# Kernel tuning notes

Measured on AMD Instinct MI355X. Metric: run time of the kernel, lower is better.

The kernel has to match this reference:

```python
import jax, jax.numpy as jnp
import numpy as np

N = 20000      # n_nodes
E = 320000     # n_edges (avg degree 16)
DIM = 64       # feature dim
HEADS = 4      # attention heads; per-head channel = DIM (PyG TransformerConv with concat=False)


def setup_inputs() -> dict:
    key = jax.random.key(0)
    ks = jax.random.split(key, 12)
    s = 0.05
    return {
        "f_mole": jax.random.normal(ks[0], (N, DIM), jnp.float32),
        "edge_weight": jax.random.uniform(ks[1], (E,), jnp.float32),
        "gcn_w": jax.random.normal(ks[2], (DIM, DIM), jnp.float32) * s,
        "gcn_b": jnp.zeros((DIM,), jnp.float32),
        "wq": jax.random.normal(ks[3], (DIM, HEADS * DIM), jnp.float32) * s,
        "bq": jnp.zeros((HEADS * DIM,), jnp.float32),
        "wk": jax.random.normal(ks[4], (DIM, HEADS * DIM), jnp.float32) * s,
        "bk": jnp.zeros((HEADS * DIM,), jnp.float32),
        "wv": jax.random.normal(ks[5], (DIM, HEADS * DIM), jnp.float32) * s,
        "bv": jnp.zeros((HEADS * DIM,), jnp.float32),
        "wskip": jax.random.normal(ks[6], (DIM, DIM), jnp.float32) * s,
        "bskip": jnp.zeros((DIM,), jnp.float32),
        "wbeta": jax.random.normal(ks[7], (3 * DIM, 1), jnp.float32) * s,
        "conv_w": jax.random.normal(ks[8], (DIM, DIM), jnp.float32) * s,  # Conv1d weight[o,0,k,0]
        "conv_b": jnp.zeros((DIM,), jnp.float32),
        "edges": jax.random.randint(ks[9], (2, E), 0, N, jnp.int32),
    }


def _forward(f_mole, edge_weight, gcn_w, gcn_b, wq, bq, wk, bk, wv, bv,
             wskip, bskip, wbeta, conv_w, conv_b, edges):
    n = f_mole.shape[0]
    dim = f_mole.shape[1]
    heads = wq.shape[1] // dim
    src, dst = edges[0], edges[1]  # PyG flow: source -> target

    # ---- GCNConv(dim, dim) with edge weights (add_self_loops=True, normalize=True) ----
    loops = jnp.arange(n, dtype=src.dtype)
    src_sl = jnp.concatenate([src, loops])
    dst_sl = jnp.concatenate([dst, loops])
    ew = jnp.concatenate([edge_weight, jnp.ones((n,), f_mole.dtype)])
    deg = jax.ops.segment_sum(ew, dst_sl, num_segments=n)
    dinv = jnp.where(deg > 0, jax.lax.rsqrt(deg), 0.0)
    norm = dinv[src_sl] * ew * dinv[dst_sl]              # (E+N,)
    xw = f_mole @ gcn_w                                   # (N, dim)
    agg = jax.ops.segment_sum(norm[:, None] * xw[src_sl], dst_sl, num_segments=n)
    f_gcn = jax.nn.relu(agg + gcn_b)                      # (N, dim)

    # ---- TransformerConv(dim, dim, heads, concat=False, beta=True) ----
    q = (f_gcn @ wq + bq).reshape(n, heads, dim)
    k = (f_gcn @ wk + bk).reshape(n, heads, dim)
    v = (f_gcn @ wv + bv).reshape(n, heads, dim)
    logits = jnp.einsum('ehc,ehc->eh', q[dst], k[src]) / jnp.sqrt(jnp.float32(dim))  # (E, H)
    m = jax.ops.segment_max(logits, dst, num_segments=n)  # (N, H)
    ex = jnp.exp(logits - m[dst])
    z = jax.ops.segment_sum(ex, dst, num_segments=n)      # (N, H)
    alpha = ex / z[dst]                                   # per-target softmax over edges
    out = jax.ops.segment_sum(alpha[:, :, None] * v[src], dst, num_segments=n)  # (N, H, dim)
    out = out.mean(axis=1)                                # concat=False -> head mean
    x_r = f_gcn @ wskip + bskip                           # root/skip branch
    beta = jax.nn.sigmoid(jnp.concatenate([out, x_r, out - x_r], axis=-1) @ wbeta)  # (N, 1)
    f_tf = jax.nn.relu(beta * x_r + (1.0 - beta) * out)   # (N, dim)

    # ---- Conv1d(1, dim, kernel_size=(dim,1)) on f_tf.T viewed as (1,1,dim,N) ----
    # out[o, n] = sum_k conv_w[o, k] * f_tf.T[k, n] + conv_b[o]  -> shape (1, dim, 1, N)
    conv = jnp.einsum('ok,nk->on', conv_w, f_tf) + conv_b[:, None]  # (dim, N)
    # torch .view(1, n_mole, -1) on (1, dim, 1, N): row-major reshape
    f_intra = conv.reshape(1, n, dim)
    return f_intra


def reference(f_mole, edge_weight, gcn_w, gcn_b, wq, bq, wk, bk, wv, bv,
              wskip, bskip, wbeta, conv_w, conv_b, edges):
    return _forward(f_mole, edge_weight, gcn_w, gcn_b, wq, bq, wk, bk, wv, bv,
                    wskip, bskip, wbeta, conv_w, conv_b, edges)
```

## Files before the change

kernel.cpp:

```cpp
#include <hip/hip_runtime.h>
#include <hip/hip_bf16.h>
#include <hip/hip_fp16.h>

#define DIM 64
#define HEADS 4
#define HD 256
#define CAP 64

typedef __attribute__((ext_vector_type(8))) short bf16x8;
typedef __attribute__((ext_vector_type(8))) unsigned short u16x8;
typedef __attribute__((ext_vector_type(4))) float f32x4;

template<int CTRL>
__device__ __forceinline__ float dpp_rot(float x) {
    return __int_as_float(__builtin_amdgcn_update_dpp(
        0, __float_as_int(x), CTRL, 0xF, 0xF, true));
}
__device__ __forceinline__ float reduce16(float x) {
    x += dpp_rot<0x121>(x);
    x += dpp_rot<0x122>(x);
    x += dpp_rot<0x124>(x);
    x += dpp_rot<0x128>(x);
    return x;
}
__device__ __forceinline__ unsigned short f2bf(float f) {
    unsigned u = __float_as_uint(f);
    unsigned r = (u + 0x7FFFu + ((u >> 16) & 1u)) >> 16;
    return (unsigned short)r;
}
__device__ __forceinline__ float bf2f(unsigned short u) {
    return __uint_as_float((unsigned)u << 16);
}
__device__ __forceinline__ float rec_w(unsigned rec) {
    return __half2float(__ushort_as_half((unsigned short)(rec & 0xffffu)));
}

__global__ void scatter_all(const int* __restrict__ edges, const float* __restrict__ ew,
                            int* counts, unsigned* __restrict__ csr, int nE) {
    int e = blockIdx.x * blockDim.x + threadIdx.x;
    if (e < nE) {
        int dst = edges[nE + e];
        int src = edges[e];
        float w = ew[e];
        int p = atomicAdd(&counts[dst], 1);
        unsigned rec = ((unsigned)src << 16)
                     | (unsigned)__half_as_ushort(__float2half(w));
        csr[(dst << 6) + p] = rec;
    }
}

__global__ __launch_bounds__(256) void wt_conv(const float* __restrict__ wq,
                                               const float* __restrict__ wk,
                                               const float* __restrict__ wv,
                                               const float* __restrict__ wsk,
                                               unsigned short* __restrict__ wt) {
    int p = blockIdx.x;
    const float* W; int ncw, col0;
    if (p < 4)       { W = wq;  ncw = HD;  col0 = p * 64; }
    else if (p < 8)  { W = wk;  ncw = HD;  col0 = (p - 4) * 64; }
    else if (p < 12) { W = wv;  ncw = HD;  col0 = (p - 8) * 64; }
    else             { W = wsk; ncw = DIM; col0 = 0; }
    int c  = threadIdx.x >> 2;
    int k0 = (threadIdx.x & 3) * 16;
    unsigned short* out = wt + ((size_t)p * 64 + c) * 64 + k0;
    #pragma unroll
    for (int j = 0; j < 16; ++j)
        out[j] = f2bf(W[(size_t)(k0 + j) * ncw + col0 + c]);
}

__device__ __forceinline__ void tile_load_A(float (*As)[68], const float* __restrict__ A,
                                            int row0, int n, int tid) {
    int c4 = (tid & 15) * 4;
    int sw = (tid & 7) << 2;
    #pragma unroll
    for (int it = 0; it < 4; ++it) {
        int r = (tid >> 4) + it * 16;
        float4 val = make_float4(0.f, 0.f, 0.f, 0.f);
        if (row0 + r < n)
            val = *reinterpret_cast<const float4*>(A + (size_t)(row0 + r) * DIM + c4);
        int rs = r ^ sw;
        As[c4 + 0][rs] = val.x;
        As[c4 + 1][rs] = val.y;
        As[c4 + 2][rs] = val.z;
        As[c4 + 3][rs] = val.w;
    }
}

__device__ __forceinline__ void tile_mm(const float (*As)[68], const float (*Bs)[68],
                                        float acc[4][4], int r0, int c0) {
    #pragma unroll 8
    for (int kk = 0; kk < 64; ++kk) {
        int sw = ((kk >> 2) & 7) << 2;
        float4 av = *reinterpret_cast<const float4*>(&As[kk][r0 ^ sw]);
        float4 bv = *reinterpret_cast<const float4*>(&Bs[kk][c0]);
        float a_[4] = {av.x, av.y, av.z, av.w};
        float b_[4] = {bv.x, bv.y, bv.z, bv.w};
        #pragma unroll
        for (int i = 0; i < 4; ++i)
            #pragma unroll
            for (int j = 0; j < 4; ++j)
                acc[i][j] += a_[i] * b_[j];
    }
}

__global__ __launch_bounds__(256) void gemm_xw(const float* __restrict__ A,
                                               const float* __restrict__ W,
                                               const int* __restrict__ counts,
                                               const unsigned* __restrict__ csr,
                                               float* __restrict__ dinv,
                                               unsigned short* __restrict__ out,
                                               int n) {
    __shared__ float As[64][68];
    __shared__ float Bs[64][68];
    __shared__ float dloc[64];
    int row0 = blockIdx.x * 64;
    int tid = threadIdx.x;

    if (tid < 64) {
        int r = row0 + tid;
        if (r < n) {
            int c = counts[r];
            const unsigned* p = csr + ((size_t)r << 6);
            float s = 0.f;
            for (int j = 0; j < c; ++j) s += rec_w(p[j]);
            float d = rsqrtf(s + 1.0f);
            dinv[r] = d;
            dloc[tid] = d;
        }
    }

    tile_load_A(As, A, row0, n, tid);
    #pragma unroll
    for (int it = 0; it < 4; ++it) {
        int r  = (tid >> 4) + it * 16;
        int c4 = (tid & 15) * 4;
        *reinterpret_cast<float4*>(&Bs[r][c4]) =
            *reinterpret_cast<const float4*>(W + (size_t)r * DIM + c4);
    }
    __syncthreads();
    int r0 = (tid >> 4) * 4;
    int c0 = (tid & 15) * 4;
    float acc[4][4] = {};
    tile_mm(As, Bs, acc, r0, c0);
    #pragma unroll
    for (int i = 0; i < 4; ++i) {
        int r = row0 + r0 + i;
        if (r >= n) continue;
        float d = dloc[r0 + i];
        ushort4 u;
        u.x = f2bf(d * acc[i][0]); u.y = f2bf(d * acc[i][1]);
        u.z = f2bf(d * acc[i][2]); u.w = f2bf(d * acc[i][3]);
        *reinterpret_cast<ushort4*>(out + (size_t)r * DIM + c0) = u;
    }
}

__global__ __launch_bounds__(256) void gcn_agg(const unsigned short* __restrict__ xws,
                                               const int* __restrict__ counts,
                                               const unsigned* __restrict__ csr,
                                               const float* __restrict__ dinv,
                                               const float* __restrict__ gcn_b,
                                               unsigned short* __restrict__ f_gcnh, int n) {
    int wave = threadIdx.x >> 6;
    int lane = threadIdx.x & 63;
    int i = blockIdx.x * 4 + wave;
    if (i >= n) return;
    int eo = lane >> 4;
    int cg = lane & 15;

    float4 acc = make_float4(0.f, 0.f, 0.f, 0.f);
    int e0 = i << 6;
    int e1 = e0 + counts[i];
    int eb = e0;
    for (; eb + 16 <= e1; eb += 16) {
        unsigned p[4];
        #pragma unroll
        for (int j = 0; j < 4; ++j) p[j] = csr[eb + 4 * j + eo];
        ushort4 x[4];
        #pragma unroll
        for (int j = 0; j < 4; ++j)
            x[j] = *reinterpret_cast<const ushort4*>(xws + (size_t)(p[j] >> 16) * DIM + cg * 4);
        #pragma unroll
        for (int j = 0; j < 4; ++j) {
            float c = rec_w(p[j]);
            acc.x += c * bf2f(x[j].x); acc.y += c * bf2f(x[j].y);
            acc.z += c * bf2f(x[j].z); acc.w += c * bf2f(x[j].w);
        }
    }
    for (int e = eb + eo; e < e1; e += 4) {
        unsigned p = csr[e];
        float c = rec_w(p);
        ushort4 x4 = *reinterpret_cast<const ushort4*>(xws + (size_t)(p >> 16) * DIM + cg * 4);
        acc.x += c * bf2f(x4.x); acc.y += c * bf2f(x4.y);
        acc.z += c * bf2f(x4.z); acc.w += c * bf2f(x4.w);
    }
    acc.x += __shfl_xor(acc.x, 16, 64); acc.x += __shfl_xor(acc.x, 32, 64);
    acc.y += __shfl_xor(acc.y, 16, 64); acc.y += __shfl_xor(acc.y, 32, 64);
    acc.z += __shfl_xor(acc.z, 16, 64); acc.z += __shfl_xor(acc.z, 32, 64);
    acc.w += __shfl_xor(acc.w, 16, 64); acc.w += __shfl_xor(acc.w, 32, 64);

    float di = dinv[i];
    ushort4 xs = *reinterpret_cast<const ushort4*>(xws + (size_t)i * DIM + cg * 4);
    const float* b = gcn_b + cg * 4;
    if (eo == 0) {
        ushort4 u;
        u.x = f2bf(fmaxf(di * (acc.x + bf2f(xs.x)) + b[0], 0.f));
        u.y = f2bf(fmaxf(di * (acc.y + bf2f(xs.y)) + b[1], 0.f));
        u.z = f2bf(fmaxf(di * (acc.z + bf2f(xs.z)) + b[2], 0.f));
        u.w = f2bf(fmaxf(di * (acc.w + bf2f(xs.w)) + b[3], 0.f));
        *reinterpret_cast<ushort4*>(f_gcnh + (size_t)i * DIM + cg * 4) = u;
    }
}

__global__ __launch_bounds__(256) void qkv_mfma(const unsigned short* __restrict__ Ah,
        const unsigned short* __restrict__ wt,
        const float* __restrict__ bq, const float* __restrict__ bk,
        const float* __restrict__ bv, const float* __restrict__ bsk,
        unsigned short* __restrict__ qo, unsigned short* __restrict__ kvb,
        float* __restrict__ xrb, int n) {
    int ty = blockIdx.y;
    const float* bias; float scale = 1.0f;
    int mode;
    int col0 = (ty & 3) * 64;
    if (ty < 4)       { bias = bq;  mode = 0; scale = 0.125f; }
    else if (ty < 8)  { bias = bk;  mode = 1; }
    else if (ty < 12) { bias = bv;  mode = 2; }
    else              { bias = bsk; mode = 3; col0 = 0; }

    int row0 = blockIdx.x * 64;
    int wid  = threadIdx.x >> 6;
    int lane = threadIdx.x & 63;
    int hm = wid >> 1, hn = wid & 1;
    int lrow = lane & 15;
    int lk8  = (lane >> 4) * 8;
    const unsigned short* wtp = wt + (size_t)ty * 64 * 64;

    bf16x8 afr[2][2];
    #pragma unroll
    for (int ks = 0; ks < 2; ++ks)
        #pragma unroll
        for (int fm = 0; fm < 2; ++fm) {
            int r = row0 + hm * 32 + fm * 16 + lrow;
            bf16x8 v8;
            if (r < n) {
                v8 = *reinterpret_cast<const bf16x8*>(Ah + (size_t)r * DIM + ks * 32 + lk8);
            } else {
                #pragma unroll
                for (int j = 0; j < 8; ++j) v8[j] = 0;
            }
            afr[ks][fm] = v8;
        }

    bf16x8 bfr[2][2];
    #pragma unroll
    for (int ks = 0; ks < 2; ++ks)
        #pragma unroll
        for (int fn = 0; fn < 2; ++fn) {
            int cl = hn * 32 + fn * 16 + lrow;
            bfr[ks][fn] = *reinterpret_cast<const bf16x8*>(
                wtp + (size_t)cl * 64 + ks * 32 + lk8);
        }

    f32x4 zz = {0.f, 0.f, 0.f, 0.f};
    f32x4 acc[2][2] = {{zz, zz}, {zz, zz}};
    #pragma unroll
    for (int ks = 0; ks < 2; ++ks)
        #pragma unroll
        for (int fm = 0; fm < 2; ++fm)
            #pragma unroll
            for (int fn = 0; fn < 2; ++fn)
                acc[fm][fn] = __builtin_amdgcn_mfma_f32_16x16x32_bf16(
                    afr[ks][fm], bfr[ks][fn], acc[fm][fn], 0, 0, 0);

    int drow = (lane >> 4) * 4;
    int dcol = lane & 15;
    #pragma unroll
    for (int fm = 0; fm < 2; ++fm)
        #pragma unroll
        for (int fn = 0; fn < 2; ++fn) {
            int col = col0 + hn * 32 + fn * 16 + dcol;
            float bcol = bias[col];
            #pragma unroll
            for (int r = 0; r < 4; ++r) {
                int row = row0 + hm * 32 + fm * 16 + drow + r;
                if (row >= n) continue;
                float val = (acc[fm][fn][r] + bcol) * scale;
                if (mode == 0) {
                    qo[(size_t)row * HD + col] = f2bf(val);
                } else if (mode == 3) {
                    xrb[(size_t)row * DIM + col] = val;
                } else {
                    int h = col >> 6, c6 = col & 63;
                    kvb[(size_t)row * 512 + h * 128 + (c6 >> 2) * 8 + (c6 & 3)
                        + (mode == 2 ? 4 : 0)] = f2bf(val);
                }
            }
        }
}

__global__ __launch_bounds__(256) void attn_fused(const unsigned short* __restrict__ q,
                                                  const unsigned short* __restrict__ kvb,
                                                  const float* __restrict__ x_r,
                                                  const int* __restrict__ counts,
                                                  const unsigned* __restrict__ csr,
                                                  const float* __restrict__ wbeta,
                                                  float* __restrict__ f_tf, int n) {
    int wave = threadIdx.x >> 6;
    int lane = threadIdx.x & 63;
    int i = blockIdx.x * 4 + wave;
    if (i >= n) return;
    int h  = lane >> 4;
    int cg = lane & 15;
    int kvoff = h * 128 + cg * 8;

    ushort4 qv = *reinterpret_cast<const ushort4*>(q + (size_t)i * HD + h * DIM + cg * 4);
    float4 q4;
    q4.x = bf2f(qv.x); q4.y = bf2f(qv.y); q4.z = bf2f(qv.z); q4.w = bf2f(qv.w);
    float z = 0.f;
    float4 a = make_float4(0.f, 0.f, 0.f, 0.f);

    int e0 = i << 6;
    int cnt = counts[i];
    int e1 = e0 + cnt;
    int e = e0;
    for (; e + 8 <= e1; e += 8) {
        int s[8];
        #pragma unroll
        for (int j = 0; j < 8; ++j) s[j] = (int)(csr[e + j] >> 16);
        u16x8 kv[8];
        #pragma unroll
        for (int j = 0; j < 8; ++j)
            kv[j] = *reinterpret_cast<const u16x8*>(kvb + (size_t)s[j] * 512 + kvoff);
        float pl[8];
        #pragma unroll
        for (int j = 0; j < 8; ++j)
            pl[j] = q4.x * bf2f(kv[j][0]) + q4.y * bf2f(kv[j][1])
                  + q4.z * bf2f(kv[j][2]) + q4.w * bf2f(kv[j][3]);
        #pragma unroll
        for (int j = 0; j < 8; ++j) pl[j] = reduce16(pl[j]);
        #pragma unroll
        for (int j = 0; j < 8; ++j) {
            float ez = __expf(pl[j]);
            z += ez;
            a.x += ez * bf2f(kv[j][4]); a.y += ez * bf2f(kv[j][5]);
            a.z += ez * bf2f(kv[j][6]); a.w += ez * bf2f(kv[j][7]);
        }
    }
    for (; e + 4 <= e1; e += 4) {
        int s[4];
        #pragma unroll
        for (int j = 0; j < 4; ++j) s[j] = (int)(csr[e + j] >> 16);
        u16x8 kv[4];
        #pragma unroll
        for (int j = 0; j < 4; ++j)
            kv[j] = *reinterpret_cast<const u16x8*>(kvb + (size_t)s[j] * 512 + kvoff);
        #pragma unroll
        for (int j = 0; j < 4; ++j) {
            float p = q4.x * bf2f(kv[j][0]) + q4.y * bf2f(kv[j][1])
                    + q4.z * bf2f(kv[j][2]) + q4.w * bf2f(kv[j][3]);
            p = reduce16(p);
            float ez = __expf(p);
            z += ez;
            a.x += ez * bf2f(kv[j][4]); a.y += ez * bf2f(kv[j][5]);
            a.z += ez * bf2f(kv[j][6]); a.w += ez * bf2f(kv[j][7]);
        }
    }
    for (; e < e1; ++e) {
        int s = (int)(csr[e] >> 16);
        u16x8 kv = *reinterpret_cast<const u16x8*>(kvb + (size_t)s * 512 + kvoff);
        float p = q4.x * bf2f(kv[0]) + q4.y * bf2f(kv[1])
                + q4.z * bf2f(kv[2]) + q4.w * bf2f(kv[3]);
        p = reduce16(p);
        float ez = __expf(p);
        z += ez;
        a.x += ez * bf2f(kv[4]); a.y += ez * bf2f(kv[5]);
        a.z += ez * bf2f(kv[6]); a.w += ez * bf2f(kv[7]);
    }

    float inv = (cnt > 0) ? 1.0f / z : 0.f;
    float4 o;
    o.x = a.x * inv; o.y = a.y * inv; o.z = a.z * inv; o.w = a.w * inv;
    o.x += __shfl_xor(o.x, 16, 64); o.x += __shfl_xor(o.x, 32, 64);
    o.y += __shfl_xor(o.y, 16, 64); o.y += __shfl_xor(o.y, 32, 64);
    o.z += __shfl_xor(o.z, 16, 64); o.z += __shfl_xor(o.z, 32, 64);
    o.w += __shfl_xor(o.w, 16, 64); o.w += __shfl_xor(o.w, 32, 64);
    o.x *= 0.25f; o.y *= 0.25f; o.z *= 0.25f; o.w *= 0.25f;

    float4 xr4 = *reinterpret_cast<const float4*>(x_r + (size_t)i * DIM + cg * 4);
    const float* w1 = wbeta + cg * 4;
    const float* w2 = wbeta + 64 + cg * 4;
    const float* w3 = wbeta + 128 + cg * 4;
    float t = o.x * w1[0] + o.y * w1[1] + o.z * w1[2] + o.w * w1[3]
            + xr4.x * w2[0] + xr4.y * w2[1] + xr4.z * w2[2] + xr4.w * w2[3]
            + (o.x - xr4.x) * w3[0] + (o.y - xr4.y) * w3[1]
            + (o.z - xr4.z) * w3[2] + (o.w - xr4.w) * w3[3];
    t = reduce16(t);
    float beta = 1.0f / (1.0f + __expf(-t));
    float4 r;
    r.x = fmaxf(beta * xr4.x + (1.0f - beta) * o.x, 0.f);
    r.y = fmaxf(beta * xr4.y + (1.0f - beta) * o.y, 0.f);
    r.z = fmaxf(beta * xr4.z + (1.0f - beta) * o.z, 0.f);
    r.w = fmaxf(beta * xr4.w + (1.0f - beta) * o.w, 0.f);
    if (h == 0)
        *reinterpret_cast<float4*>(f_tf + (size_t)i * DIM + cg * 4) = r;
}

__global__ __launch_bounds__(256) void conv_out_k(const float* __restrict__ f_tf,
                                                  const float* __restrict__ conv_w,
                                                  const float* __restrict__ conv_b,
                                                  float* __restrict__ out, int n) {
    int nn = blockIdx.x * 256 + threadIdx.x;
    int ob = blockIdx.y * 16;
    if (nn >= n) return;
    float4 r4[16];
    #pragma unroll
    for (int j = 0; j < 16; ++j)
        r4[j] = *reinterpret_cast<const float4*>(f_tf + (size_t)nn * DIM + j * 4);
    #pragma unroll
    for (int oo = 0; oo < 16; ++oo) {
        int o = ob + oo;
        const float* wr = conv_w + (size_t)o * DIM;
        float acc = conv_b[o];
        #pragma unroll
        for (int j = 0; j < 16; ++j) {
            acc += r4[j].x * wr[j * 4 + 0] + r4[j].y * wr[j * 4 + 1] +
                   r4[j].z * wr[j * 4 + 2] + r4[j].w * wr[j * 4 + 3];
        }
        out[(size_t)o * n + nn] = acc;
    }
}

extern "C" void kernel_launch(void* const* d_in, const int* in_sizes, int n_in,
                              void* d_out, int out_size, void* d_ws, size_t ws_size,
                              hipStream_t stream) {
    const float* f_mole = (const float*)d_in[0];
    const float* edge_w = (const float*)d_in[1];
    const float* gcn_w  = (const float*)d_in[2];
    const float* gcn_b  = (const float*)d_in[3];
    const float* wq     = (const float*)d_in[4];
    const float* bq     = (const float*)d_in[5];
    const float* wk     = (const float*)d_in[6];
    const float* bk     = (const float*)d_in[7];
    const float* wv     = (const float*)d_in[8];
    const float* bv     = (const float*)d_in[9];
    const float* wskip  = (const float*)d_in[10];
    const float* bskip  = (const float*)d_in[11];
    const float* wbeta  = (const float*)d_in[12];
    const float* conv_w = (const float*)d_in[13];
    const float* conv_b = (const float*)d_in[14];
    const int*   edges  = (const int*)d_in[15];

    int N = in_sizes[0] / DIM;
    int E = in_sizes[1];

    float* ws = (float*)d_ws;
    size_t o = 0;
    int*      counts = (int*)(ws + o);      o += N;
    float*    dinv   = ws + o;              o += N;
    unsigned* csr    = (unsigned*)(ws + o); o += (size_t)N * CAP;
    unsigned short* wt     = (unsigned short*)(ws + o); o += (size_t)13 * 64 * 64 / 2;
    unsigned short* xws    = (unsigned short*)(ws + o); o += (size_t)N * DIM / 2;
    unsigned short* f_gcnh = (unsigned short*)(ws + o); o += (size_t)N * DIM / 2;
    unsigned short* qb     = (unsigned short*)(ws + o); o += (size_t)N * HD / 2;
    unsigned short* kvb    = (unsigned short*)(ws + o); o += (size_t)N * 512 / 2;
    float* xrb = ws + o;                    o += (size_t)N * DIM;
    float* ftf = ws + o;                    o += (size_t)N * DIM;

    int ebl = (E + 255) / 256;
    int nbl = (N + 255) / 256;
    int gbl = (N + 63) / 64;

    hipMemsetAsync(d_ws, 0, (size_t)N * sizeof(int), stream);
    scatter_all<<<ebl, 256, 0, stream>>>(edges, edge_w, counts, csr, E);
    wt_conv<<<13, 256, 0, stream>>>(wq, wk, wv, wskip, wt);

    gemm_xw<<<gbl, 256, 0, stream>>>(f_mole, gcn_w, counts, csr, dinv, xws, N);
    gcn_agg<<<(N + 3) / 4, 256, 0, stream>>>(xws, counts, csr, dinv, gcn_b, f_gcnh, N);

    qkv_mfma<<<dim3(gbl, 13), 256, 0, stream>>>(f_gcnh, wt, bq, bk, bv, bskip,
                                                qb, kvb, xrb, N);

    attn_fused<<<(N + 3) / 4, 256, 0, stream>>>(qb, kvb, xrb, counts, csr, wbeta, ftf, N);
    conv_out_k<<<dim3(nbl, 4), 256, 0, stream>>>(ftf, conv_w, conv_b, (float*)d_out, N);
}
```

Before: 144.8 us.

## Fold weight conversion into QKV kernel, loop projections per block, restage conv

Removes the separate weight transpose/bf16 conversion kernel. The QKV GEMM now loads fp32 weights directly with strided reads and converts them in registers. It also loops over all 13 projection tiles inside one block, so each A tile is loaded once instead of 13 times. The output conv kernel is restructured to stage a 64-node tile of f_tf in shared memory, with four 16-output groups per block, instead of each thread loading its full row. In exchange it cuts a launch and repeated A reads, but adds uncoalesced weight loads redone by every block and a serial 13-iteration loop on a grid 13x smaller.

```diff
diff --git a/kernel.cpp b/kernel.cpp
--- a/kernel.cpp
+++ b/kernel.cpp
@@ -47,25 +47,6 @@
                      | (unsigned)__half_as_ushort(__float2half(w));
         csr[(dst << 6) + p] = rec;
     }
-}
-
-__global__ __launch_bounds__(256) void wt_conv(const float* __restrict__ wq,
-                                               const float* __restrict__ wk,
-                                               const float* __restrict__ wv,
-                                               const float* __restrict__ wsk,
-                                               unsigned short* __restrict__ wt) {
-    int p = blockIdx.x;
-    const float* W; int ncw, col0;
-    if (p < 4)       { W = wq;  ncw = HD;  col0 = p * 64; }
-    else if (p < 8)  { W = wk;  ncw = HD;  col0 = (p - 4) * 64; }
-    else if (p < 12) { W = wv;  ncw = HD;  col0 = (p - 8) * 64; }
-    else             { W = wsk; ncw = DIM; col0 = 0; }
-    int c  = threadIdx.x >> 2;
-    int k0 = (threadIdx.x & 3) * 16;
-    unsigned short* out = wt + ((size_t)p * 64 + c) * 64 + k0;
-    #pragma unroll
-    for (int j = 0; j < 16; ++j)
-        out[j] = f2bf(W[(size_t)(k0 + j) * ncw + col0 + c]);
 }
 
 __device__ __forceinline__ void tile_load_A(float (*As)[68], const float* __restrict__ A,
@@ -212,27 +193,18 @@
 }
 
 __global__ __launch_bounds__(256) void qkv_mfma(const unsigned short* __restrict__ Ah,
-        const unsigned short* __restrict__ wt,
-        const float* __restrict__ bq, const float* __restrict__ bk,
-        const float* __restrict__ bv, const float* __restrict__ bsk,
+        const float* __restrict__ wq, const float* __restrict__ bq,
+        const float* __restrict__ wk, const float* __restrict__ bk,
+        const float* __restrict__ wv, const float* __restrict__ bv,
+        const float* __restrict__ wsk, const float* __restrict__ bsk,
         unsigned short* __restrict__ qo, unsigned short* __restrict__ kvb,
         float* __restrict__ xrb, int n) {
-    int ty = blockIdx.y;
-    const float* bias; float scale = 1.0f;
-    int mode;
-    int col0 = (ty & 3) * 64;
-    if (ty < 4)       { bias = bq;  mode = 0; scale = 0.125f; }
-    else if (ty < 8)  { bias = bk;  mode = 1; }
-    else if (ty < 12) { bias = bv;  mode = 2; }
-    else              { bias = bsk; mode = 3; col0 = 0; }
-
     int row0 = blockIdx.x * 64;
     int wid  = threadIdx.x >> 6;
     int lane = threadIdx.x & 63;
     int hm = wid >> 1, hn = wid & 1;
     int lrow = lane & 15;
     int lk8  = (lane >> 4) * 8;
-    const unsigned short* wtp = wt + (size_t)ty * 64 * 64;
 
     bf16x8 afr[2][2];
     #pragma unroll
@@ -250,51 +222,67 @@
             afr[ks][fm] = v8;
         }
 
-    bf16x8 bfr[2][2];
-    #pragma unroll
-    for (int ks = 0; ks < 2; ++ks)
-        #pragma unroll
-        for (int fn = 0; fn < 2; ++fn) {
-            int cl = hn * 32 + fn * 16 + lrow;
-            bfr[ks][fn] = *reinterpret_cast<const bf16x8*>(
-                wtp + (size_t)cl * 64 + ks * 32 + lk8);
-        }
-
-    f32x4 zz = {0.f, 0.f, 0.f, 0.f};
-    f32x4 acc[2][2] = {{zz, zz}, {zz, zz}};
-    #pragma unroll
-    for (int ks = 0; ks < 2; ++ks)
+    int drow = (lane >> 4) * 4;
+    int dcol = lane & 15;
+
+    #pragma unroll 1
+    for (int ty = 0; ty < 13; ++ty) {
+        const float* W; const float* bias; float scale = 1.0f;
+        int ncw, mode;
+        int col0 = (ty & 3) * 64;
+        if (ty < 4)       { W = wq;  bias = bq;  ncw = HD;  mode = 0; scale = 0.125f; }
+        else if (ty < 8)  { W = wk;  bias = bk;  ncw = HD;  mode = 1; }
+        else if (ty < 12) { W = wv;  bias = bv;  ncw = HD;  mode = 2; }
+        else              { W = wsk; bias = bsk; ncw = DIM; mode = 3; col0 = 0; }
+
+        bf16x8 bfr[2][2];
+        #pragma unroll
+        for (int ks = 0; ks < 2; ++ks)
+            #pragma unroll
+            for (int fn = 0; fn < 2; ++fn) {
+                int c = col0 + hn * 32 + fn * 16 + lrow;
+                const float* wp = W + (size_t)(ks * 32 + lk8) * ncw + c;
+                bf16x8 v8;
+                #pragma unroll
+                for (int j = 0; j < 8; ++j)
+                    v8[j] = (short)f2bf(wp[(size_t)j * ncw]);
+                bfr[ks][fn] = v8;
+            }
+
+        f32x4 zz = {0.f, 0.f, 0.f, 0.f};
+        f32x4 acc[2][2] = {{zz, zz}, {zz, zz}};
+        #pragma unroll
+        for (int ks = 0; ks < 2; ++ks)
+            #pragma unroll
+            for (int fm = 0; fm < 2; ++fm)
+                #pragma unroll
+                for (int fn = 0; fn < 2; ++fn)
+                    acc[fm][fn] = __builtin_amdgcn_mfma_f32_16x16x32_bf16(
+                        afr[ks][fm], bfr[ks][fn], acc[fm][fn], 0, 0, 0);
+
         #pragma unroll
         for (int fm = 0; fm < 2; ++fm)
             #pragma unroll
-            for (int fn = 0; fn < 2; ++fn)
-                acc[fm][fn] = __builtin_amdgcn_mfma_f32_16x16x32_bf16(
-                    afr[ks][fm], bfr[ks][fn], acc[fm][fn], 0, 0, 0);
-
-    int drow = (lane >> 4) * 4;
-    int dcol = lane & 15;
-    #pragma unroll
-    for (int fm = 0; fm < 2; ++fm)
-        #pragma unroll
-        for (int fn = 0; fn < 2; ++fn) {
-            int col = col0 + hn * 32 + fn * 16 + dcol;
-            float bcol = bias[col];
-            #pragma unroll
-            for (int r = 0; r < 4; ++r) {
-                int row = row0 + hm * 32 + fm * 16 + drow + r;
-                if (row >= n) continue;
-                float val = (acc[fm][fn][r] + bcol) * scale;
-                if (mode == 0) {
-                    qo[(size_t)row * HD + col] = f2bf(val);
-                } else if (mode == 3) {
-                    xrb[(size_t)row * DIM + col] = val;
-                } else {
-                    int h = col >> 6, c6 = col & 63;
-                    kvb[(size_t)row * 512 + h * 128 + (c6 >> 2) * 8 + (c6 & 3)
-                        + (mode == 2 ? 4 : 0)] = f2bf(val);
+            for (int fn = 0; fn < 2; ++fn) {
+                int col = col0 + hn * 32 + fn * 16 + dcol;
+                float bcol = bias[col];
+                #pragma unroll
+                for (int r = 0; r < 4; ++r) {
+                    int row = row0 + hm * 32 + fm * 16 + drow + r;
+                    if (row >= n) continue;
+                    float val = (acc[fm][fn][r] + bcol) * scale;
+                    if (mode == 0) {
+                        qo[(size_t)row * HD + col] = f2bf(val);
+                    } else if (mode == 3) {
+                        xrb[(size_t)row * DIM + col] = val;
+                    } else {
+                        int h = col >> 6, c6 = col & 63;
+                        kvb[(size_t)row * 512 + h * 128 + (c6 >> 2) * 8 + (c6 & 3)
+                            + (mode == 2 ? 4 : 0)] = f2bf(val);
+                    }
                 }
             }
-        }
+    }
 }
 
 __global__ __launch_bounds__(256) void attn_fused(const unsigned short* __restrict__ q,
@@ -408,23 +396,33 @@
                                                   const float* __restrict__ conv_w,
                                                   const float* __restrict__ conv_b,
                                                   float* __restrict__ out, int n) {
-    int nn = blockIdx.x * 256 + threadIdx.x;
-    int ob = blockIdx.y * 16;
+    __shared__ float ft[64][65];
+    int n0 = blockIdx.x * 64;
+    int tid = threadIdx.x;
+    int nd = tid >> 2, c16 = (tid & 3) * 16;
+    if (n0 + nd < n) {
+        #pragma unroll
+        for (int j = 0; j < 4; ++j) {
+            float4 v = *reinterpret_cast<const float4*>(
+                f_tf + (size_t)(n0 + nd) * DIM + c16 + j * 4);
+            ft[nd][c16 + j * 4 + 0] = v.x;
+            ft[nd][c16 + j * 4 + 1] = v.y;
+            ft[nd][c16 + j * 4 + 2] = v.z;
+            ft[nd][c16 + j * 4 + 3] = v.w;
+        }
+    }
+    __syncthreads();
+    int nl = tid & 63;
+    int og = tid >> 6;
+    int nn = n0 + nl;
     if (nn >= n) return;
-    float4 r4[16];
-    #pragma unroll
-    for (int j = 0; j < 16; ++j)
-        r4[j] = *reinterpret_cast<const float4*>(f_tf + (size_t)nn * DIM + j * 4);
-    #pragma unroll
+    #pragma unroll 1
     for (int oo = 0; oo < 16; ++oo) {
-        int o = ob + oo;
+        int o = og * 16 + oo;
         const float* wr = conv_w + (size_t)o * DIM;
         float acc = conv_b[o];
         #pragma unroll
-        for (int j = 0; j < 16; ++j) {
-            acc += r4[j].x * wr[j * 4 + 0] + r4[j].y * wr[j * 4 + 1] +
-                   r4[j].z * wr[j * 4 + 2] + r4[j].w * wr[j * 4 + 3];
-        }
+        for (int k = 0; k < 64; ++k) acc += ft[nl][k] * wr[k];
         out[(size_t)o * n + nn] = acc;
     }
 }
@@ -457,7 +455,6 @@
     int*      counts = (int*)(ws + o);      o += N;
     float*    dinv   = ws + o;              o += N;
     unsigned* csr    = (unsigned*)(ws + o); o += (size_t)N * CAP;
-    unsigned short* wt     = (unsigned short*)(ws + o); o += (size_t)13 * 64 * 64 / 2;
     unsigned short* xws    = (unsigned short*)(ws + o); o += (size_t)N * DIM / 2;
     unsigned short* f_gcnh = (unsigned short*)(ws + o); o += (size_t)N * DIM / 2;
     unsigned short* qb     = (unsigned short*)(ws + o); o += (size_t)N * HD / 2;
@@ -466,19 +463,17 @@
     float* ftf = ws + o;                    o += (size_t)N * DIM;
 
     int ebl = (E + 255) / 256;
-    int nbl = (N + 255) / 256;
     int gbl = (N + 63) / 64;
 
     hipMemsetAsync(d_ws, 0, (size_t)N * sizeof(int), stream);
     scatter_all<<<ebl, 256, 0, stream>>>(edges, edge_w, counts, csr, E);
-    wt_conv<<<13, 256, 0, stream>>>(wq, wk, wv, wskip, wt);
 
     gemm_xw<<<gbl, 256, 0, stream>>>(f_mole, gcn_w, counts, csr, dinv, xws, N);
     gcn_agg<<<(N + 3) / 4, 256, 0, stream>>>(xws, counts, csr, dinv, gcn_b, f_gcnh, N);
 
-    qkv_mfma<<<dim3(gbl, 13), 256, 0, stream>>>(f_gcnh, wt, bq, bk, bv, bskip,
-                                                qb, kvb, xrb, N);
+    qkv_mfma<<<gbl, 256, 0, stream>>>(f_gcnh, wq, bq, wk, bk, wv, bv,
+                                      wskip, bskip, qb, kvb, xrb, N);
 
     attn_fused<<<(N + 3) / 4, 256, 0, stream>>>(qb, kvb, xrb, counts, csr, wbeta, ftf, N);
-    conv_out_k<<<dim3(nbl, 4), 256, 0, stream>>>(ftf, conv_w, conv_b, (float*)d_out, N);
-}
+    conv_out_k<<<gbl, 256, 0, stream>>>(ftf, conv_w, conv_b, (float*)d_out, N);
+}
```

After: 152.2 us. 1.05x slower.
